# Optimization experiments

Measured on AMD Instinct MI355X. Metric: run time of the kernel, lower is better.

Reference implementation:

```python
import jax, jax.numpy as jnp
import numpy as np

T, H, E, K = 16384, 2880, 128, 4

def setup_inputs() -> dict:
    key = jax.random.key(0)
    k1, k2, k3 = jax.random.split(key, 3)
    return {
        "hidden_states": jax.random.normal(k1, (T, H), dtype=jnp.float32),
        "weight": jax.random.normal(k2, (E, H), dtype=jnp.float32) * 0.02,
        "bias": jax.random.normal(k3, (E,), dtype=jnp.float32) * 0.02,
    }

def reference(hidden_states, weight, bias):
    x = hidden_states.reshape(-1, weight.shape[1])            # [T, H]
    logits = jnp.einsum('th,eh->te', x, weight) + bias        # [T, E]
    top_val, top_idx = jax.lax.top_k(logits, K)               # sorted desc, [T, K]
    top_val = jax.nn.softmax(top_val, axis=-1)
    rows = jnp.arange(logits.shape[0])[:, None]
    scores = jnp.zeros_like(logits).at[rows, top_idx].set(top_val)
    return scores, top_idx
```

## Files before the change

kernel.cpp:

```cpp
#include <hip/hip_runtime.h>
#include <math.h>


#define T_TOK 16384
#define HDIM  2880
#define EEXP  128
#define KTOP  4

#define TM   32
#define NT   256
#define KC   64
#define NCH  (HDIM / KC)
#define XBUF 8192
#define TAU  2.5e-4f

typedef __attribute__((ext_vector_type(8))) short bf16x8;
typedef __attribute__((ext_vector_type(4))) float f32x4;

#define MFMA(a, b, c) __builtin_amdgcn_mfma_f32_16x16x32_bf16((a), (b), (c), 0, 0, 0)

__global__ __launch_bounds__(256) void w_split(
    const float* __restrict__ w, char* __restrict__ wp)
{
    const int gid  = blockIdx.x * 256 + threadIdx.x;
    const int lane = gid & 63;
    const int q    = gid >> 6;
    const int ks   = q & 1;
    const int q2   = q >> 1;
    const int c    = q2 % NCH;
    const int F    = q2 / NCH;
    const int e    = F * 16 + (lane & 15);
    const int k0   = c * 64 + ks * 32 + (lane >> 4) * 8;

    const float* src = w + (size_t)e * HDIM + k0;
    float4 v0 = *(const float4*)(src);
    float4 v1 = *(const float4*)(src + 4);
    float vv[8] = {v0.x, v0.y, v0.z, v0.w, v1.x, v1.y, v1.z, v1.w};
    union { unsigned short s[8]; uint4 u; } H, L;
#pragma unroll
    for (int j = 0; j < 8; ++j) {
        unsigned u = __float_as_uint(vv[j]);
        H.s[j] = (unsigned short)(u >> 16);
        float rr = vv[j] - __uint_as_float(u & 0xffff0000u);
        L.s[j] = (unsigned short)(__float_as_uint(rr) >> 16);
    }
    const int tile = ((F * NCH + c) * 2 + ks) * 2;
    *(uint4*)(wp + (size_t)tile * 1024 + lane * 16)       = H.u;
    *(uint4*)(wp + (size_t)(tile + 1) * 1024 + lane * 16) = L.u;
}

static __device__ __forceinline__ void split_write256(char* base, int off, float4 v) {
    union { float4 v4; unsigned u[4]; } uv; uv.v4 = v;
    unsigned h01 = __builtin_amdgcn_perm(uv.u[1], uv.u[0], 0x07060302u);
    unsigned h23 = __builtin_amdgcn_perm(uv.u[3], uv.u[2], 0x07060302u);
    float r0 = v.x - __uint_as_float(uv.u[0] & 0xffff0000u);
    float r1 = v.y - __uint_as_float(uv.u[1] & 0xffff0000u);
    float r2 = v.z - __uint_as_float(uv.u[2] & 0xffff0000u);
    float r3 = v.w - __uint_as_float(uv.u[3] & 0xffff0000u);
    unsigned l01 = __builtin_amdgcn_perm(__float_as_uint(r1), __float_as_uint(r0), 0x07060302u);
    unsigned l23 = __builtin_amdgcn_perm(__float_as_uint(r3), __float_as_uint(r2), 0x07060302u);
    uint2 hw; hw.x = h01; hw.y = h23;
    uint2 lw; lw.x = l01; lw.y = l23;
    *(uint2*)(base + off)       = hw;
    *(uint2*)(base + off + 128) = lw;
}

__global__ __launch_bounds__(NT, 2) void router_fused(
    const float* __restrict__ x, const char* __restrict__ wp,
    const float* __restrict__ w, const float* __restrict__ bias,
    float* __restrict__ out)
{
    __shared__ char smem[3 * XBUF];
    const int tid  = threadIdx.x;
    const int tok0 = blockIdx.x * TM;
    const int lane = tid & 63;
    const int wv   = tid >> 6;
    const int r    = lane & 15;
    const int g    = lane >> 4;

    char* xb0 = smem;
    char* xb1 = smem + XBUF;
    char* xb2 = smem + 2 * XBUF;

    int xoff[2];
    const float* xptr[2];
#pragma unroll
    for (int i = 0; i < 2; ++i) {
        int f = tid + i * NT;
        int row = f >> 4, c4 = f & 15;
        xoff[i] = row * 256 + ((((c4 >> 1) ^ (row & 7)) << 4) | ((c4 & 1) << 3));
        xptr[i] = x + (size_t)(tok0 + row) * HDIM + c4 * 4;
    }

    int aoff[2][2];
#pragma unroll
    for (int tf = 0; tf < 2; ++tf) {
        int row = tf * 16 + r;
#pragma unroll
        for (int ks = 0; ks < 2; ++ks)
            aoff[tf][ks] = row * 256 + (((ks * 4 + g) ^ (row & 7)) << 4);
    }

    f32x4 a00 = {0.f, 0.f, 0.f, 0.f}, a01 = a00, a10 = a00, a11 = a00;

#define LOADX(pf, cc) do {                                            \
        pf[0] = *(const float4*)(xptr[0] + (cc) * KC);                \
        pf[1] = *(const float4*)(xptr[1] + (cc) * KC); } while (0)

#define WRITEX(pf, bb) do {                                           \
        split_write256((bb), xoff[0], pf[0]);                         \
        split_write256((bb), xoff[1], pf[1]); } while (0)

#define LOADW(W, cc) do {                                             \
        _Pragma("unroll")                                             \
        for (int F2 = 0; F2 < 2; ++F2)                                \
        _Pragma("unroll")                                             \
        for (int ks_ = 0; ks_ < 2; ++ks_)                             \
        _Pragma("unroll")                                             \
        for (int p_ = 0; p_ < 2; ++p_)                                \
            W[F2*4 + ks_*2 + p_] = *(const bf16x8*)(wp +              \
                (size_t)((((wv*2 + F2) * NCH + (cc)) * 2 + ks_) * 2 + p_) * 1024 \
                + lane * 16); } while (0)

#define MFMA_CHUNK(cb, W) do {                                        \
        _Pragma("unroll")                                             \
        for (int ks_ = 0; ks_ < 2; ++ks_) {                           \
            bf16x8 ah0 = *(const bf16x8*)((cb) + aoff[0][ks_]);       \
            bf16x8 al0 = *(const bf16x8*)((cb) + aoff[0][ks_] + 128); \
            bf16x8 ah1 = *(const bf16x8*)((cb) + aoff[1][ks_]);       \
            bf16x8 al1 = *(const bf16x8*)((cb) + aoff[1][ks_] + 128); \
            bf16x8 bh0 = W[ks_*2],     bl0 = W[ks_*2 + 1];            \
            bf16x8 bh1 = W[4 + ks_*2], bl1 = W[4 + ks_*2 + 1];        \
            a00 = MFMA(ah0, bh0, a00); a01 = MFMA(ah0, bh1, a01);     \
            a10 = MFMA(ah1, bh0, a10); a11 = MFMA(ah1, bh1, a11);     \
            a00 = MFMA(ah0, bl0, a00); a01 = MFMA(ah0, bl1, a01);     \
            a10 = MFMA(ah1, bl0, a10); a11 = MFMA(ah1, bl1, a11);     \
            a00 = MFMA(al0, bh0, a00); a01 = MFMA(al0, bh1, a01);     \
            a10 = MFMA(al1, bh0, a10); a11 = MFMA(al1, bh1, a11);     \
        } } while (0)

    float4 pfA[2], pfB[2], pfC[2];
    bf16x8 wA[8], wB[8], wC[8];

    LOADX(pfA, 0); LOADX(pfB, 1); LOADX(pfC, 2);
    LOADW(wA, 0); LOADW(wB, 1);
    WRITEX(pfA, xb0);
    __syncthreads();

    for (int c = 0; c < NCH; c += 3) {
        if (c + 3 < NCH) LOADX(pfA, c + 3);
        LOADW(wC, c + 2);
        MFMA_CHUNK(xb0, wA);
        WRITEX(pfB, xb1);
        __syncthreads();
        if (c + 3 < NCH) LOADW(wA, c + 3);
        if (c + 4 < NCH) LOADX(pfB, c + 4);
        MFMA_CHUNK(xb1, wB);
        WRITEX(pfC, xb2);
        __syncthreads();
        if (c + 4 < NCH) LOADW(wB, c + 4);
        if (c + 5 < NCH) LOADX(pfC, c + 5);
        MFMA_CHUNK(xb2, wC);
        if (c + 3 < NCH) WRITEX(pfA, xb0);
        __syncthreads();
    }

    float* logitsL = (float*)smem;
    const float bv0 = bias[wv * 32 + r];
    const float bv1 = bias[wv * 32 + 16 + r];
#pragma unroll
    for (int q = 0; q < 4; ++q) {
        int m0 = g * 4 + q, m1 = m0 + 16;
        int e0 = wv * 32 + r, e1 = e0 + 16;
        logitsL[m0 * 130 + e0] = a00[q] + bv0;
        logitsL[m0 * 130 + e1] = a01[q] + bv1;
        logitsL[m1 * 130 + e0] = a10[q] + bv0;
        logitsL[m1 * 130 + e1] = a11[q] + bv1;
    }
    float*  cvf = (float*) (smem + 16640);
    int*    cie = (int*)   (smem + 17664);
    int*    flg = (int*)   (smem + 18688);
    double* svd = (double*)(smem + 18816);
    int*    sid = (int*)   (smem + 19840);
    double* cvd = (double*)(smem + 20352);
    __syncthreads();

    {
        const int t = tid >> 3, s = tid & 7;
        float v[8]; int id[8];
#pragma unroll
        for (int k = 0; k < 8; ++k) { v[k] = -3.4e38f; id[k] = 0x7fffffff; }
        for (int jj = 0; jj < 16; ++jj) {
            float lv = logitsL[t * 130 + s * 16 + jj];
            int   e  = s * 16 + jj;
            bool gt[8];
#pragma unroll
            for (int k = 0; k < 8; ++k)
                gt[k] = (lv > v[k]) || (lv == v[k] && e < id[k]);
#pragma unroll
            for (int k = 7; k >= 1; --k)
                if (gt[k - 1]) { v[k] = v[k - 1]; id[k] = id[k - 1]; }
#pragma unroll
            for (int k = 0; k < 8; ++k) {
                bool put = gt[k] && (k == 0 || !gt[k - 1]);
                if (put) { v[k] = lv; id[k] = e; }
            }
        }
#pragma unroll
        for (int rd = 0; rd < 8; ++rd) {
            float hv = v[0]; int hi = id[0];
#pragma unroll
            for (int off = 1; off < 8; off <<= 1) {
                float ov = __shfl_xor(hv, off);
                int   oi = __shfl_xor(hi, off);
                if (ov > hv || (ov == hv && oi < hi)) { hv = ov; hi = oi; }
            }
            if (s == 0) { cvf[t * 8 + rd] = hv; cie[t * 8 + rd] = hi; }
            bool mine = (v[0] == hv) && (id[0] == hi);
            if (mine) {
#pragma unroll
                for (int k = 0; k < 7; ++k) { v[k] = v[k + 1]; id[k] = id[k + 1]; }
                v[7] = -3.4e38f; id[7] = 0x7fffffff;
            }
        }
    }
    __syncthreads();

    if (tid < TM) {
        float gmin = 3.4e38f;
#pragma unroll
        for (int k = 0; k < 4; ++k)
            gmin = fminf(gmin, cvf[tid * 8 + k] - cvf[tid * 8 + k + 1]);
        flg[tid] = (gmin < TAU);
    }
    if (tid < 128) {
        int t2 = tid >> 2, k = tid & 3;
        svd[t2 * 4 + k] = (double)cvf[t2 * 8 + k];
        sid[t2 * 4 + k] = cie[t2 * 8 + k];
    }
    __syncthreads();

    for (int ts = 0; ts < TM; ++ts) {
        if (!flg[ts]) continue;
#pragma unroll
        for (int h2 = 0; h2 < 2; ++h2) {
            const int cand = wv * 2 + h2;
            const int ce = cie[ts * 8 + cand];
            const float4* xr = (const float4*)(x + (size_t)(tok0 + ts) * HDIM);
            const float4* wr = (const float4*)(w + (size_t)ce * HDIM);
            double q0 = 0.0, q1 = 0.0, q2 = 0.0, q3 = 0.0;
            for (int i2 = 0; i2 < 12; ++i2) {
                int fi = lane + i2 * 64;
                if (fi < HDIM / 4) {
                    float4 xv = xr[fi];
                    float4 wv4 = wr[fi];
                    q0 = fma((double)xv.x, (double)wv4.x, q0);
                    q1 = fma((double)xv.y, (double)wv4.y, q1);
                    q2 = fma((double)xv.z, (double)wv4.z, q2);
                    q3 = fma((double)xv.w, (double)wv4.w, q3);
                }
            }
            double accd = (q0 + q2) + (q1 + q3);
#pragma unroll
            for (int off = 32; off > 0; off >>= 1)
                accd += __shfl_xor(accd, off);
            if (lane == 0) cvd[cand] = accd + (double)bias[ce];
        }
        __syncthreads();
        if (tid < 8) {
            double mv = cvd[tid]; int mi2 = cie[ts * 8 + tid];
            int rk = 0;
#pragma unroll
            for (int j2 = 0; j2 < 8; ++j2) {
                double oj = cvd[j2];
                rk += (oj > mv) || (oj == mv && cie[ts * 8 + j2] < mi2);
            }
            if (rk < 4) { svd[ts * 4 + rk] = mv; sid[ts * 4 + rk] = mi2; }
        }
        __syncthreads();
    }

    float* srow = (float*)smem;
    float4 z4 = make_float4(0.f, 0.f, 0.f, 0.f);
#pragma unroll
    for (int i = 0; i < 4; ++i)
        ((float4*)srow)[tid + i * NT] = z4;
    __syncthreads();

    if (tid < TM) {
        double m  = svd[tid * 4];
        double e0 = exp(svd[tid * 4 + 0] - m), e1 = exp(svd[tid * 4 + 1] - m);
        double e2 = exp(svd[tid * 4 + 2] - m), e3 = exp(svd[tid * 4 + 3] - m);
        double inv = 1.0 / ((e0 + e1) + (e2 + e3));
        float* oidx = out + (size_t)T_TOK * EEXP + (size_t)(tok0 + tid) * KTOP;
        int i0 = sid[tid * 4 + 0], i1 = sid[tid * 4 + 1];
        int i2 = sid[tid * 4 + 2], i3 = sid[tid * 4 + 3];
        oidx[0] = (float)i0; oidx[1] = (float)i1;
        oidx[2] = (float)i2; oidx[3] = (float)i3;
        srow[tid * EEXP + i0] = (float)(e0 * inv);
        srow[tid * EEXP + i1] = (float)(e1 * inv);
        srow[tid * EEXP + i2] = (float)(e2 * inv);
        srow[tid * EEXP + i3] = (float)(e3 * inv);
    }
    __syncthreads();

    float4* orow = (float4*)(out + (size_t)tok0 * EEXP);
#pragma unroll
    for (int i = 0; i < 4; ++i)
        orow[tid + i * NT] = ((float4*)srow)[tid + i * NT];
}

extern "C" void kernel_launch(void* const* d_in, const int* in_sizes, int n_in,
                              void* d_out, int out_size, void* d_ws, size_t ws_size,
                              hipStream_t stream) {
    const float* x    = (const float*)d_in[0];
    const float* w    = (const float*)d_in[1];
    const float* bias = (const float*)d_in[2];
    float* out        = (float*)d_out;
    char*  wp         = (char*)d_ws;

    hipLaunchKernelGGL(w_split, dim3(180), dim3(256), 0, stream, w, wp);
    hipLaunchKernelGGL(router_fused, dim3(T_TOK / TM), dim3(NT), 0, stream,
                       x, wp, w, bias, out);
}
```

Baseline: 80.22 us.

## Switch router GEMM to 32x32x16 bf16 MFMA with matching weight layout

Replaces the four 16x16x32 MFMA accumulators per wave with one 32x32x16 accumulator covering 32 tokens by 32 experts. The pre-split weight layout, the LDS A-fragment offsets and the logits write-out are reworked to fit the new instruction shape. The aim is fewer MFMA issues and LDS A-fragment loads per chunk, since each A fragment is reused across a full 32-wide expert tile. The larger MFMA has longer latency and one dependent accumulator chain, so there is less instruction-level parallelism to hide it.

```diff
diff --git a/kernel.cpp b/kernel.cpp
--- a/kernel.cpp
+++ b/kernel.cpp
@@ -11,13 +11,15 @@
 #define NT   256
 #define KC   64
 #define NCH  (HDIM / KC)
+#define NT16 (HDIM / 16)
 #define XBUF 8192
 #define TAU  2.5e-4f
 
-typedef __attribute__((ext_vector_type(8))) short bf16x8;
-typedef __attribute__((ext_vector_type(4))) float f32x4;
-
-#define MFMA(a, b, c) __builtin_amdgcn_mfma_f32_16x16x32_bf16((a), (b), (c), 0, 0, 0)
+typedef __attribute__((ext_vector_type(8)))  short bf16x8;
+typedef __attribute__((ext_vector_type(4)))  float f32x4;
+typedef __attribute__((ext_vector_type(16))) float f32x16;
+
+#define MFMA32(a, b, c) __builtin_amdgcn_mfma_f32_32x32x16_bf16((a), (b), (c), 0, 0, 0)
 
 __global__ __launch_bounds__(256) void w_split(
     const float* __restrict__ w, char* __restrict__ wp)
@@ -25,12 +27,10 @@
     const int gid  = blockIdx.x * 256 + threadIdx.x;
     const int lane = gid & 63;
     const int q    = gid >> 6;
-    const int ks   = q & 1;
-    const int q2   = q >> 1;
-    const int c    = q2 % NCH;
-    const int F    = q2 / NCH;
-    const int e    = F * 16 + (lane & 15);
-    const int k0   = c * 64 + ks * 32 + (lane >> 4) * 8;
+    const int t    = q % NT16;
+    const int F2   = q / NT16;
+    const int e    = F2 * 32 + (lane & 31);
+    const int k0   = t * 16 + (lane >> 5) * 8;
 
     const float* src = w + (size_t)e * HDIM + k0;
     float4 v0 = *(const float4*)(src);
@@ -44,7 +44,7 @@
         float rr = vv[j] - __uint_as_float(u & 0xffff0000u);
         L.s[j] = (unsigned short)(__float_as_uint(rr) >> 16);
     }
-    const int tile = ((F * NCH + c) * 2 + ks) * 2;
+    const int tile = (F2 * NT16 + t) * 2;
     *(uint4*)(wp + (size_t)tile * 1024 + lane * 16)       = H.u;
     *(uint4*)(wp + (size_t)(tile + 1) * 1024 + lane * 16) = L.u;
 }
@@ -75,8 +75,6 @@
     const int tok0 = blockIdx.x * TM;
     const int lane = tid & 63;
     const int wv   = tid >> 6;
-    const int r    = lane & 15;
-    const int g    = lane >> 4;
 
     char* xb0 = smem;
     char* xb1 = smem + XBUF;
@@ -92,16 +90,17 @@
         xptr[i] = x + (size_t)(tok0 + row) * HDIM + c4 * 4;
     }
 
-    int aoff[2][2];
-#pragma unroll
-    for (int tf = 0; tf < 2; ++tf) {
-        int row = tf * 16 + r;
-#pragma unroll
-        for (int ks = 0; ks < 2; ++ks)
-            aoff[tf][ks] = row * 256 + (((ks * 4 + g) ^ (row & 7)) << 4);
-    }
-
-    f32x4 a00 = {0.f, 0.f, 0.f, 0.f}, a01 = a00, a10 = a00, a11 = a00;
+    int aof[4];
+    {
+        int row = lane & 31;
+#pragma unroll
+        for (int ks = 0; ks < 4; ++ks)
+            aof[ks] = row * 256 + (((ks * 2 + (lane >> 5)) ^ (row & 7)) << 4);
+    }
+
+    f32x16 acc;
+#pragma unroll
+    for (int i = 0; i < 16; ++i) acc[i] = 0.f;
 
 #define LOADX(pf, cc) do {                                            \
         pf[0] = *(const float4*)(xptr[0] + (cc) * KC);                \
@@ -113,30 +112,21 @@
 
 #define LOADW(W, cc) do {                                             \
         _Pragma("unroll")                                             \
-        for (int F2 = 0; F2 < 2; ++F2)                                \
-        _Pragma("unroll")                                             \
-        for (int ks_ = 0; ks_ < 2; ++ks_)                             \
+        for (int ks_ = 0; ks_ < 4; ++ks_)                             \
         _Pragma("unroll")                                             \
         for (int p_ = 0; p_ < 2; ++p_)                                \
-            W[F2*4 + ks_*2 + p_] = *(const bf16x8*)(wp +              \
-                (size_t)((((wv*2 + F2) * NCH + (cc)) * 2 + ks_) * 2 + p_) * 1024 \
+            W[ks_*2 + p_] = *(const bf16x8*)(wp +                     \
+                (size_t)((wv * NT16 + (cc) * 4 + ks_) * 2 + p_) * 1024 \
                 + lane * 16); } while (0)
 
 #define MFMA_CHUNK(cb, W) do {                                        \
         _Pragma("unroll")                                             \
-        for (int ks_ = 0; ks_ < 2; ++ks_) {                           \
-            bf16x8 ah0 = *(const bf16x8*)((cb) + aoff[0][ks_]);       \
-            bf16x8 al0 = *(const bf16x8*)((cb) + aoff[0][ks_] + 128); \
-            bf16x8 ah1 = *(const bf16x8*)((cb) + aoff[1][ks_]);       \
-            bf16x8 al1 = *(const bf16x8*)((cb) + aoff[1][ks_] + 128); \
-            bf16x8 bh0 = W[ks_*2],     bl0 = W[ks_*2 + 1];            \
-            bf16x8 bh1 = W[4 + ks_*2], bl1 = W[4 + ks_*2 + 1];        \
-            a00 = MFMA(ah0, bh0, a00); a01 = MFMA(ah0, bh1, a01);     \
-            a10 = MFMA(ah1, bh0, a10); a11 = MFMA(ah1, bh1, a11);     \
-            a00 = MFMA(ah0, bl0, a00); a01 = MFMA(ah0, bl1, a01);     \
-            a10 = MFMA(ah1, bl0, a10); a11 = MFMA(ah1, bl1, a11);     \
-            a00 = MFMA(al0, bh0, a00); a01 = MFMA(al0, bh1, a01);     \
-            a10 = MFMA(al1, bh0, a10); a11 = MFMA(al1, bh1, a11);     \
+        for (int ks_ = 0; ks_ < 4; ++ks_) {                           \
+            bf16x8 ah = *(const bf16x8*)((cb) + aof[ks_]);            \
+            bf16x8 al = *(const bf16x8*)((cb) + aof[ks_] + 128);      \
+            acc = MFMA32(ah, W[ks_*2],     acc);                      \
+            acc = MFMA32(ah, W[ks_*2 + 1], acc);                      \
+            acc = MFMA32(al, W[ks_*2],     acc);                      \
         } } while (0)
 
     float4 pfA[2], pfB[2], pfC[2];
@@ -166,16 +156,14 @@
     }
 
     float* logitsL = (float*)smem;
-    const float bv0 = bias[wv * 32 + r];
-    const float bv1 = bias[wv * 32 + 16 + r];
-#pragma unroll
-    for (int q = 0; q < 4; ++q) {
-        int m0 = g * 4 + q, m1 = m0 + 16;
-        int e0 = wv * 32 + r, e1 = e0 + 16;
-        logitsL[m0 * 130 + e0] = a00[q] + bv0;
-        logitsL[m0 * 130 + e1] = a01[q] + bv1;
-        logitsL[m1 * 130 + e0] = a10[q] + bv0;
-        logitsL[m1 * 130 + e1] = a11[q] + bv1;
+    {
+        const int e  = wv * 32 + (lane & 31);
+        const float bv = bias[e];
+#pragma unroll
+        for (int i = 0; i < 16; ++i) {
+            int tok = (i & 3) + 8 * (i >> 2) + 4 * (lane >> 5);
+            logitsL[tok * 130 + e] = acc[i] + bv;
+        }
     }
     float*  cvf = (float*) (smem + 16640);
     int*    cie = (int*)   (smem + 17664);
```

Result: no change. 81.76 us (+1.9%).

## Double token tile to 64 rows and use 8 waves each owning 16 experts

Applied to the files above, without the earlier changes.

Raises the per-block token tile from 32 to 64 and threads from 256 to 512. Each wave now handles 16 experts across 4 token fragments instead of 32 experts across 2. The split-bf16 weight fragments are loaded once per block for twice as many tokens, which halves global weight traffic per token. In exchange the block uses twice the LDS and more threads, which may cut occupancy, and the grid gets half as many blocks.

```diff
diff --git a/kernel.cpp b/kernel.cpp
--- a/kernel.cpp
+++ b/kernel.cpp
@@ -7,11 +7,11 @@
 #define EEXP  128
 #define KTOP  4
 
-#define TM   32
-#define NT   256
+#define TM   64
+#define NT   512
 #define KC   64
 #define NCH  (HDIM / KC)
-#define XBUF 8192
+#define XBUF 16384
 #define TAU  2.5e-4f
 
 typedef __attribute__((ext_vector_type(8))) short bf16x8;
@@ -92,16 +92,19 @@
         xptr[i] = x + (size_t)(tok0 + row) * HDIM + c4 * 4;
     }
 
-    int aoff[2][2];
-#pragma unroll
-    for (int tf = 0; tf < 2; ++tf) {
+    int aoff[4][2];
+#pragma unroll
+    for (int tf = 0; tf < 4; ++tf) {
         int row = tf * 16 + r;
 #pragma unroll
         for (int ks = 0; ks < 2; ++ks)
             aoff[tf][ks] = row * 256 + (((ks * 4 + g) ^ (row & 7)) << 4);
     }
 
-    f32x4 a00 = {0.f, 0.f, 0.f, 0.f}, a01 = a00, a10 = a00, a11 = a00;
+    f32x4 acc[4];
+    const f32x4 zf = {0.f, 0.f, 0.f, 0.f};
+#pragma unroll
+    for (int tf = 0; tf < 4; ++tf) acc[tf] = zf;
 
 #define LOADX(pf, cc) do {                                            \
         pf[0] = *(const float4*)(xptr[0] + (cc) * KC);                \
@@ -112,35 +115,30 @@
         split_write256((bb), xoff[1], pf[1]); } while (0)
 
 #define LOADW(W, cc) do {                                             \
-        _Pragma("unroll")                                             \
-        for (int F2 = 0; F2 < 2; ++F2)                                \
         _Pragma("unroll")                                             \
         for (int ks_ = 0; ks_ < 2; ++ks_)                             \
         _Pragma("unroll")                                             \
         for (int p_ = 0; p_ < 2; ++p_)                                \
-            W[F2*4 + ks_*2 + p_] = *(const bf16x8*)(wp +              \
-                (size_t)((((wv*2 + F2) * NCH + (cc)) * 2 + ks_) * 2 + p_) * 1024 \
+            W[ks_*2 + p_] = *(const bf16x8*)(wp +                     \
+                (size_t)(((wv * NCH + (cc)) * 2 + ks_) * 2 + p_) * 1024 \
                 + lane * 16); } while (0)
 
 #define MFMA_CHUNK(cb, W) do {                                        \
         _Pragma("unroll")                                             \
         for (int ks_ = 0; ks_ < 2; ++ks_) {                           \
-            bf16x8 ah0 = *(const bf16x8*)((cb) + aoff[0][ks_]);       \
-            bf16x8 al0 = *(const bf16x8*)((cb) + aoff[0][ks_] + 128); \
-            bf16x8 ah1 = *(const bf16x8*)((cb) + aoff[1][ks_]);       \
-            bf16x8 al1 = *(const bf16x8*)((cb) + aoff[1][ks_] + 128); \
-            bf16x8 bh0 = W[ks_*2],     bl0 = W[ks_*2 + 1];            \
-            bf16x8 bh1 = W[4 + ks_*2], bl1 = W[4 + ks_*2 + 1];        \
-            a00 = MFMA(ah0, bh0, a00); a01 = MFMA(ah0, bh1, a01);     \
-            a10 = MFMA(ah1, bh0, a10); a11 = MFMA(ah1, bh1, a11);     \
-            a00 = MFMA(ah0, bl0, a00); a01 = MFMA(ah0, bl1, a01);     \
-            a10 = MFMA(ah1, bl0, a10); a11 = MFMA(ah1, bl1, a11);     \
-            a00 = MFMA(al0, bh0, a00); a01 = MFMA(al0, bh1, a01);     \
-            a10 = MFMA(al1, bh0, a10); a11 = MFMA(al1, bh1, a11);     \
+            bf16x8 bh = W[ks_*2], bl = W[ks_*2 + 1];                  \
+            _Pragma("unroll")                                         \
+            for (int tf_ = 0; tf_ < 4; ++tf_) {                       \
+                bf16x8 ah = *(const bf16x8*)((cb) + aoff[tf_][ks_]);  \
+                bf16x8 al = *(const bf16x8*)((cb) + aoff[tf_][ks_] + 128); \
+                acc[tf_] = MFMA(ah, bh, acc[tf_]);                    \
+                acc[tf_] = MFMA(ah, bl, acc[tf_]);                    \
+                acc[tf_] = MFMA(al, bh, acc[tf_]);                    \
+            }                                                         \
         } } while (0)
 
     float4 pfA[2], pfB[2], pfC[2];
-    bf16x8 wA[8], wB[8], wC[8];
+    bf16x8 wA[4], wB[4], wC[4];
 
     LOADX(pfA, 0); LOADX(pfB, 1); LOADX(pfC, 2);
     LOADW(wA, 0); LOADW(wB, 1);
@@ -166,23 +164,23 @@
     }
 
     float* logitsL = (float*)smem;
-    const float bv0 = bias[wv * 32 + r];
-    const float bv1 = bias[wv * 32 + 16 + r];
-#pragma unroll
-    for (int q = 0; q < 4; ++q) {
-        int m0 = g * 4 + q, m1 = m0 + 16;
-        int e0 = wv * 32 + r, e1 = e0 + 16;
-        logitsL[m0 * 130 + e0] = a00[q] + bv0;
-        logitsL[m0 * 130 + e1] = a01[q] + bv1;
-        logitsL[m1 * 130 + e0] = a10[q] + bv0;
-        logitsL[m1 * 130 + e1] = a11[q] + bv1;
-    }
-    float*  cvf = (float*) (smem + 16640);
-    int*    cie = (int*)   (smem + 17664);
-    int*    flg = (int*)   (smem + 18688);
-    double* svd = (double*)(smem + 18816);
-    int*    sid = (int*)   (smem + 19840);
-    double* cvd = (double*)(smem + 20352);
+    {
+        const int e  = wv * 16 + r;
+        const float bv = bias[e];
+#pragma unroll
+        for (int tf = 0; tf < 4; ++tf)
+#pragma unroll
+            for (int q = 0; q < 4; ++q) {
+                int tok = tf * 16 + g * 4 + q;
+                logitsL[tok * 130 + e] = acc[tf][q] + bv;
+            }
+    }
+    float*  cvf = (float*) (smem + 33280);
+    int*    cie = (int*)   (smem + 35328);
+    int*    flg = (int*)   (smem + 37376);
+    double* svd = (double*)(smem + 37632);
+    int*    sid = (int*)   (smem + 39680);
+    double* cvd = (double*)(smem + 40704);
     __syncthreads();
 
     {
@@ -233,7 +231,7 @@
             gmin = fminf(gmin, cvf[tid * 8 + k] - cvf[tid * 8 + k + 1]);
         flg[tid] = (gmin < TAU);
     }
-    if (tid < 128) {
+    if (tid < 256) {
         int t2 = tid >> 2, k = tid & 3;
         svd[t2 * 4 + k] = (double)cvf[t2 * 8 + k];
         sid[t2 * 4 + k] = cie[t2 * 8 + k];
@@ -242,10 +240,8 @@
 
     for (int ts = 0; ts < TM; ++ts) {
         if (!flg[ts]) continue;
-#pragma unroll
-        for (int h2 = 0; h2 < 2; ++h2) {
-            const int cand = wv * 2 + h2;
-            const int ce = cie[ts * 8 + cand];
+        {
+            const int ce = cie[ts * 8 + wv];
             const float4* xr = (const float4*)(x + (size_t)(tok0 + ts) * HDIM);
             const float4* wr = (const float4*)(w + (size_t)ce * HDIM);
             double q0 = 0.0, q1 = 0.0, q2 = 0.0, q3 = 0.0;
@@ -264,7 +260,7 @@
 #pragma unroll
             for (int off = 32; off > 0; off >>= 1)
                 accd += __shfl_xor(accd, off);
-            if (lane == 0) cvd[cand] = accd + (double)bias[ce];
+            if (lane == 0) cvd[wv] = accd + (double)bias[ce];
         }
         __syncthreads();
         if (tid < 8) {
```

After: 82.04 us. 2.3% more time.

## Replace split-bf16 three-pass MFMA with single-pass fp16 MFMA

Applied to the files above, without the earlier changes.

Replaces the hi/lo bf16 split emulation of fp32 (three MFMAs per product) with one fp16 conversion and a single f16 MFMA per product. This halves the LDS footprint per staged x chunk and the packed weight size, and cuts MFMA count by three times. It raises the top-k tie tolerance TAU to cover the larger fp16 rounding error. The risk is reduced accuracy: selection near ties relies on the fallback refinement path shown by TAU.

```diff
diff --git a/kernel.cpp b/kernel.cpp
--- a/kernel.cpp
+++ b/kernel.cpp
@@ -11,15 +11,15 @@
 #define NT   256
 #define KC   64
 #define NCH  (HDIM / KC)
-#define XBUF 8192
-#define TAU  2.5e-4f
-
-typedef __attribute__((ext_vector_type(8))) short bf16x8;
-typedef __attribute__((ext_vector_type(4))) float f32x4;
-
-#define MFMA(a, b, c) __builtin_amdgcn_mfma_f32_16x16x32_bf16((a), (b), (c), 0, 0, 0)
-
-__global__ __launch_bounds__(256) void w_split(
+#define XBUF 4096
+#define TAU  4e-3f
+
+typedef __attribute__((ext_vector_type(8))) _Float16 f16x8;
+typedef __attribute__((ext_vector_type(4))) float    f32x4;
+
+#define MFMA(a, b, c) __builtin_amdgcn_mfma_f32_16x16x32_f16((a), (b), (c), 0, 0, 0)
+
+__global__ __launch_bounds__(256) void w_cvt(
     const float* __restrict__ w, char* __restrict__ wp)
 {
     const int gid  = blockIdx.x * 256 + threadIdx.x;
@@ -35,34 +35,20 @@
     const float* src = w + (size_t)e * HDIM + k0;
     float4 v0 = *(const float4*)(src);
     float4 v1 = *(const float4*)(src + 4);
-    float vv[8] = {v0.x, v0.y, v0.z, v0.w, v1.x, v1.y, v1.z, v1.w};
-    union { unsigned short s[8]; uint4 u; } H, L;
-#pragma unroll
-    for (int j = 0; j < 8; ++j) {
-        unsigned u = __float_as_uint(vv[j]);
-        H.s[j] = (unsigned short)(u >> 16);
-        float rr = vv[j] - __uint_as_float(u & 0xffff0000u);
-        L.s[j] = (unsigned short)(__float_as_uint(rr) >> 16);
-    }
-    const int tile = ((F * NCH + c) * 2 + ks) * 2;
-    *(uint4*)(wp + (size_t)tile * 1024 + lane * 16)       = H.u;
-    *(uint4*)(wp + (size_t)(tile + 1) * 1024 + lane * 16) = L.u;
+    union { _Float16 h[8]; uint4 u; } H;
+    H.h[0] = (_Float16)v0.x; H.h[1] = (_Float16)v0.y;
+    H.h[2] = (_Float16)v0.z; H.h[3] = (_Float16)v0.w;
+    H.h[4] = (_Float16)v1.x; H.h[5] = (_Float16)v1.y;
+    H.h[6] = (_Float16)v1.z; H.h[7] = (_Float16)v1.w;
+    const int tile = (F * NCH + c) * 2 + ks;
+    *(uint4*)(wp + (size_t)tile * 1024 + lane * 16) = H.u;
 }
 
-static __device__ __forceinline__ void split_write256(char* base, int off, float4 v) {
-    union { float4 v4; unsigned u[4]; } uv; uv.v4 = v;
-    unsigned h01 = __builtin_amdgcn_perm(uv.u[1], uv.u[0], 0x07060302u);
-    unsigned h23 = __builtin_amdgcn_perm(uv.u[3], uv.u[2], 0x07060302u);
-    float r0 = v.x - __uint_as_float(uv.u[0] & 0xffff0000u);
-    float r1 = v.y - __uint_as_float(uv.u[1] & 0xffff0000u);
-    float r2 = v.z - __uint_as_float(uv.u[2] & 0xffff0000u);
-    float r3 = v.w - __uint_as_float(uv.u[3] & 0xffff0000u);
-    unsigned l01 = __builtin_amdgcn_perm(__float_as_uint(r1), __float_as_uint(r0), 0x07060302u);
-    unsigned l23 = __builtin_amdgcn_perm(__float_as_uint(r3), __float_as_uint(r2), 0x07060302u);
-    uint2 hw; hw.x = h01; hw.y = h23;
-    uint2 lw; lw.x = l01; lw.y = l23;
-    *(uint2*)(base + off)       = hw;
-    *(uint2*)(base + off + 128) = lw;
+static __device__ __forceinline__ void cvt_write128(char* base, int off, float4 v) {
+    union { _Float16 h[4]; uint2 u; } U;
+    U.h[0] = (_Float16)v.x; U.h[1] = (_Float16)v.y;
+    U.h[2] = (_Float16)v.z; U.h[3] = (_Float16)v.w;
+    *(uint2*)(base + off) = U.u;
 }
 
 __global__ __launch_bounds__(NT, 2) void router_fused(
@@ -70,7 +56,7 @@
     const float* __restrict__ w, const float* __restrict__ bias,
     float* __restrict__ out)
 {
-    __shared__ char smem[3 * XBUF];
+    __shared__ char smem[20480];
     const int tid  = threadIdx.x;
     const int tok0 = blockIdx.x * TM;
     const int lane = tid & 63;
@@ -88,7 +74,7 @@
     for (int i = 0; i < 2; ++i) {
         int f = tid + i * NT;
         int row = f >> 4, c4 = f & 15;
-        xoff[i] = row * 256 + ((((c4 >> 1) ^ (row & 7)) << 4) | ((c4 & 1) << 3));
+        xoff[i] = row * 128 + ((((c4 >> 1) ^ (row & 7)) << 4) | ((c4 & 1) << 3));
         xptr[i] = x + (size_t)(tok0 + row) * HDIM + c4 * 4;
     }
 
@@ -98,7 +84,7 @@
         int row = tf * 16 + r;
 #pragma unroll
         for (int ks = 0; ks < 2; ++ks)
-            aoff[tf][ks] = row * 256 + (((ks * 4 + g) ^ (row & 7)) << 4);
+            aoff[tf][ks] = row * 128 + (((ks * 4 + g) ^ (row & 7)) << 4);
     }
 
     f32x4 a00 = {0.f, 0.f, 0.f, 0.f}, a01 = a00, a10 = a00, a11 = a00;
@@ -108,39 +94,31 @@
         pf[1] = *(const float4*)(xptr[1] + (cc) * KC); } while (0)
 
 #define WRITEX(pf, bb) do {                                           \
-        split_write256((bb), xoff[0], pf[0]);                         \
-        split_write256((bb), xoff[1], pf[1]); } while (0)
+        cvt_write128((bb), xoff[0], pf[0]);                           \
+        cvt_write128((bb), xoff[1], pf[1]); } while (0)
 
 #define LOADW(W, cc) do {                                             \
         _Pragma("unroll")                                             \
         for (int F2 = 0; F2 < 2; ++F2)                                \
         _Pragma("unroll")                                             \
         for (int ks_ = 0; ks_ < 2; ++ks_)                             \
-        _Pragma("unroll")                                             \
-        for (int p_ = 0; p_ < 2; ++p_)                                \
-            W[F2*4 + ks_*2 + p_] = *(const bf16x8*)(wp +              \
-                (size_t)((((wv*2 + F2) * NCH + (cc)) * 2 + ks_) * 2 + p_) * 1024 \
+            W[F2*2 + ks_] = *(const f16x8*)(wp +                      \
+                (size_t)(((wv*2 + F2) * NCH + (cc)) * 2 + ks_) * 1024 \
                 + lane * 16); } while (0)
 
 #define MFMA_CHUNK(cb, W) do {                                        \
         _Pragma("unroll")                                             \
         for (int ks_ = 0; ks_ < 2; ++ks_) {                           \
-            bf16x8 ah0 = *(const bf16x8*)((cb) + aoff[0][ks_]);       \
-            bf16x8 al0 = *(const bf16x8*)((cb) + aoff[0][ks_] + 128); \
-            bf16x8 ah1 = *(const bf16x8*)((cb) + aoff[1][ks_]);       \
-            bf16x8 al1 = *(const bf16x8*)((cb) + aoff[1][ks_] + 128); \
-            bf16x8 bh0 = W[ks_*2],     bl0 = W[ks_*2 + 1];            \
-            bf16x8 bh1 = W[4 + ks_*2], bl1 = W[4 + ks_*2 + 1];        \
-            a00 = MFMA(ah0, bh0, a00); a01 = MFMA(ah0, bh1, a01);     \
-            a10 = MFMA(ah1, bh0, a10); a11 = MFMA(ah1, bh1, a11);     \
-            a00 = MFMA(ah0, bl0, a00); a01 = MFMA(ah0, bl1, a01);     \
-            a10 = MFMA(ah1, bl0, a10); a11 = MFMA(ah1, bl1, a11);     \
-            a00 = MFMA(al0, bh0, a00); a01 = MFMA(al0, bh1, a01);     \
-            a10 = MFMA(al1, bh0, a10); a11 = MFMA(al1, bh1, a11);     \
+            f16x8 a0 = *(const f16x8*)((cb) + aoff[0][ks_]);          \
+            f16x8 a1 = *(const f16x8*)((cb) + aoff[1][ks_]);          \
+            a00 = MFMA(a0, W[ks_],     a00);                          \
+            a01 = MFMA(a0, W[2 + ks_], a01);                          \
+            a10 = MFMA(a1, W[ks_],     a10);                          \
+            a11 = MFMA(a1, W[2 + ks_], a11);                          \
         } } while (0)
 
     float4 pfA[2], pfB[2], pfC[2];
-    bf16x8 wA[8], wB[8], wC[8];
+    f16x8 wA[4], wB[4], wC[4];
 
     LOADX(pfA, 0); LOADX(pfB, 1); LOADX(pfC, 2);
     LOADW(wA, 0); LOADW(wB, 1);
@@ -319,7 +297,7 @@
     float* out        = (float*)d_out;
     char*  wp         = (char*)d_ws;
 
-    hipLaunchKernelGGL(w_split, dim3(180), dim3(256), 0, stream, w, wp);
+    hipLaunchKernelGGL(w_cvt, dim3(180), dim3(256), 0, stream, w, wp);
     hipLaunchKernelGGL(router_fused, dim3(T_TOK / TM), dim3(NT), 0, stream,
                        x, wp, w, bias, out);
 }
```

Measured after the change: 79.23 us, median of 3. Within noise of the previous version (-1.2%).
